# Performance work log

Measured on AMD Instinct MI355X. Metric: run time of the kernel, lower is better.

Reference implementation:

```python
import math
import jax, jax.numpy as jnp
import numpy as np

EPS = 1e-5
NUM_HEADER = 2


def pos_encoding(C, T, dtype):
    i = jnp.arange(C)
    exp = -((i - (i % 2)).astype(dtype) / C)
    freqs = jnp.power(jnp.asarray(10000.0, dtype), exp)[:, None]      # [C,1]
    phases = ((i % 2).astype(dtype) * (np.pi / 2))[:, None]           # [C,1]
    pos = jnp.arange(T, dtype=dtype)[None, :]                         # [1,T]
    return jnp.sin(pos * freqs + phases)                              # [C,T]


def layernorm2d(x, g, b):
    # LayerNorm over (C,T) jointly, per batch element (nn.LayerNorm([C, length]))
    mu = jnp.mean(x, axis=(1, 2), keepdims=True)
    var = jnp.mean((x - mu) ** 2, axis=(1, 2), keepdims=True)
    return (x - mu) * jax.lax.rsqrt(var + EPS) * g[None] + b[None]


def dsconv(x, dw_w, dw_b, pw_w, pw_b):
    # depthwise conv1d (groups=C, 'same' padding for odd k) + pointwise 1x1
    C = x.shape[1]
    k = dw_w.shape[-1]
    y = jax.lax.conv_general_dilated(
        x, dw_w[:, None, :], (1,), [(k // 2, k // 2)],
        dimension_numbers=('NCH', 'OIH', 'NCH'), feature_group_count=C)
    y = y + dw_b[None, :, None]
    y = jnp.einsum('bct,oc->bot', y, pw_w) + pw_b[None, :, None]
    return y


def attention(x, mask, Wq, Wk, Wv, Wo):
    # Faithful to source bug: all heads use Wqs[1]/Wks[1]/Wvs[1] -> identical heads.
    xt = jnp.transpose(x, (0, 2, 1))          # [B,T,C]
    C = xt.shape[-1]
    dk = C / NUM_HEADER
    q = xt @ Wq                               # [B,T,dk]
    k_ = xt @ Wk
    v = xt @ Wv
    s = jnp.einsum('bqd,bkd->bqk', q, k_) * (1.0 / math.sqrt(dk))
    hmask = mask[:, None, :]                  # mask over keys
    s = s * hmask + (1 - hmask) * (-1e30)
    a = jax.nn.softmax(s, axis=2) * mask[:, :, None]
    head = a @ v                              # [B,T,dk]
    heads = jnp.tile(head, (1, 1, NUM_HEADER))  # concat of identical heads
    out = heads @ Wo                          # [B,T,C]
    return jnp.transpose(out, (0, 2, 1))      # [B,C,T]


def setup_inputs() -> dict:
    key = jax.random.key(0)
    B, C, T = 16, 128, 1024
    NCONV, K = 4, 7
    dk = C // NUM_HEADER
    ks = jax.random.split(key, 12)
    inp = {
        'x': jax.random.normal(ks[0], (B, C, T), jnp.float32),
        'mask': jnp.ones((B, T), jnp.float32),
        'dw_w': jax.random.normal(ks[1], (NCONV, C, K), jnp.float32) * math.sqrt(2.0 / K),
        'dw_b': jnp.zeros((NCONV, C), jnp.float32),
        'pw_w': jax.random.normal(ks[2], (NCONV, C, C), jnp.float32) * math.sqrt(2.0 / C),
        'pw_b': jnp.zeros((NCONV, C), jnp.float32),
        'norm0_g': jnp.ones((C, T), jnp.float32),
        'norm0_b': jnp.zeros((C, T), jnp.float32),
        'norms_g': jnp.ones((NCONV, C, T), jnp.float32),
        'norms_b': jnp.zeros((NCONV, C, T), jnp.float32),
        'norme_g': jnp.ones((C, T), jnp.float32),
        'norme_b': jnp.zeros((C, T), jnp.float32),
        'Wq': jax.random.normal(ks[3], (C, dk), jnp.float32) * math.sqrt(2.0 / (C + dk)),
        'Wk': jax.random.normal(ks[4], (C, dk), jnp.float32) * math.sqrt(2.0 / (C + dk)),
        'Wv': jax.random.normal(ks[5], (C, dk), jnp.float32) * math.sqrt(2.0 / (C + dk)),
        'Wo': jax.random.normal(ks[6], (C, C), jnp.float32) * math.sqrt(2.0 / C),
        'fc_w': jax.random.normal(ks[7], (C, C), jnp.float32) * (0.1 * math.sqrt(6.0 / (2 * C))),
        'fc_b': jnp.zeros((C,), jnp.float32),
    }
    return inp


def reference(x, mask, dw_w, dw_b, pw_w, pw_b, norm0_g, norm0_b,
              norms_g, norms_b, norme_g, norme_b,
              Wq, Wk, Wv, Wo, fc_w, fc_b):
    B, C, T = x.shape
    nconv = dw_w.shape[0]
    # dropout is identity in eval mode (reference is deterministic)
    out = x + pos_encoding(C, T, x.dtype)[None]
    res = layernorm2d(out, norm0_g, norm0_b)
    for i in range(nconv):
        out = dsconv(out, dw_w[i], dw_b[i], pw_w[i], pw_b[i])
        out = jax.nn.relu(out)
        out = out + res
        res = out
        out = layernorm2d(out, norms_g[i], norms_b[i])
    out = attention(out, mask, Wq, Wk, Wv, Wo)
    out = out + res
    res = out
    out = layernorm2d(out, norme_g, norme_b)
    out = jnp.einsum('bct,oc->bot', out, fc_w) + fc_b[None, :, None]
    out = jax.nn.relu(out)
    out = out + res
    return out
```

## Files before the change

kernel.cpp:

```cpp
#include <hip/hip_runtime.h>
#include <math.h>

#define BB 16
#define CC 128
#define TT 1024
#define KK 7
#define DK 64
#define NSPLIT 4

typedef float f32x4 __attribute__((ext_vector_type(4)));
typedef short s16x8 __attribute__((ext_vector_type(8)));

__device__ inline short f2bf(float f) {
  union { float f; unsigned u; } v; v.f = f;
  unsigned r = (v.u + 0x7FFFu + ((v.u >> 16) & 1u)) >> 16;
  return (short)r;
}
__device__ inline float bf2f(short s) {
  union { unsigned u; float f; } v;
  v.u = ((unsigned)(unsigned short)s) << 16;
  return v.f;
}

__device__ inline void block_partial_256(float s, float ss, float* dst) {
#pragma unroll
  for (int off = 32; off; off >>= 1) { s += __shfl_xor(s, off); ss += __shfl_xor(ss, off); }
  __shared__ float red[8];
  int w = threadIdx.x >> 6;
  if ((threadIdx.x & 63) == 0) { red[2 * w] = s; red[2 * w + 1] = ss; }
  __syncthreads();
  if (threadIdx.x == 0) {
    for (int i = 1; i < 4; ++i) { s += red[2 * i]; ss += red[2 * i + 1]; }
    dst[0] = s; dst[1] = ss;
  }
}

__device__ inline void ln_stats_from_parts(const float* part_batch, int n, float* sh) {
  if (threadIdx.x < 64) {
    float s = 0.f, ss = 0.f;
    for (int i = threadIdx.x; i < n; i += 64) { s += part_batch[2 * i]; ss += part_batch[2 * i + 1]; }
#pragma unroll
    for (int off = 32; off; off >>= 1) { s += __shfl_xor(s, off); ss += __shfl_xor(ss, off); }
    if (threadIdx.x == 0) {
      const float invN = 1.f / (float)(CC * TT);
      float mu = s * invN;
      sh[0] = mu;
      sh[1] = rsqrtf(ss * invN - mu * mu + 1e-5f);
    }
  }
  __syncthreads();
}

__global__ __launch_bounds__(256) void k_prep_addpos(const float* __restrict__ x,
                                                     const float* __restrict__ pww,
                                                     const float* __restrict__ Wq,
                                                     const float* __restrict__ Wk,
                                                     const float* __restrict__ Wv,
                                                     const float* __restrict__ Wo,
                                                     const float* __restrict__ fcw,
                                                     const float* __restrict__ n0g,
                                                     const float* __restrict__ n0b,
                                                     const float* __restrict__ nsg,
                                                     const float* __restrict__ nsb,
                                                     const float* __restrict__ neg_,
                                                     const float* __restrict__ neb,
                                                     short* __restrict__ out,
                                                     float* __restrict__ part,
                                                     short* __restrict__ pwwb,
                                                     short* __restrict__ wqkvb,
                                                     short* __restrict__ wo2b,
                                                     short* __restrict__ fcwb,
                                                     short* __restrict__ lnpb) {
  if (blockIdx.x < BB * CC) {
    int bc = blockIdx.x;
    int c = bc & (CC - 1);
    float ce = (float)(c & ~1);
    float freq = expf(-(ce / (float)CC) * 9.210340371976184f);
    float phase = (c & 1) ? 1.5707963267948966f : 0.0f;
    const float4* xr = (const float4*)(x + (size_t)bc * TT);
    short* orow = out + (size_t)bc * TT;
    int t = threadIdx.x * 4;
    float4 xv = xr[threadIdx.x];
    float v0 = xv.x + sinf((float)t * freq + phase);
    float v1 = xv.y + sinf((float)(t + 1) * freq + phase);
    float v2 = xv.z + sinf((float)(t + 2) * freq + phase);
    float v3 = xv.w + sinf((float)(t + 3) * freq + phase);
    float s = v0 + v1 + v2 + v3;
    float ss = v0 * v0 + v1 * v1 + v2 * v2 + v3 * v3;
    short4 o; o.x = f2bf(v0); o.y = f2bf(v1); o.z = f2bf(v2); o.w = f2bf(v3);
    *(short4*)(orow + t) = o;
    block_partial_256(s, ss, part + (size_t)bc * 2);
    return;
  }
  int i = (blockIdx.x - BB * CC) * 256 + threadIdx.x;
  if (i < 65536) { pwwb[i] = f2bf(pww[i]); return; }
  i -= 65536;
  if (i < 24576) {
    int m = i >> 7, c = i & 127;
    int sel = m >> 6, d = m & 63;
    const float* srcp = sel == 0 ? Wq : (sel == 1 ? Wk : Wv);
    wqkvb[i] = f2bf(srcp[c * DK + d]);
    return;
  }
  i -= 24576;
  if (i < 8192) {
    int o = i >> 6, d = i & 63;
    wo2b[i] = f2bf(Wo[d * CC + o] + Wo[(d + 64) * CC + o]);
    return;
  }
  i -= 8192;
  if (i < 16384) { fcwb[i] = f2bf(fcw[i]); return; }
  i -= 16384;
  if (i >= 1572864) return;
  const int CT = CC * TT;
  float v;
  if (i < CT) v = n0g[i];
  else if (i < 2 * CT) v = n0b[i - CT];
  else if (i < 6 * CT) v = nsg[i - 2 * CT];
  else if (i < 10 * CT) v = nsb[i - 6 * CT];
  else if (i < 11 * CT) v = neg_[i - 10 * CT];
  else v = neb[i - 11 * CT];
  lnpb[i] = f2bf(v);
}

template <bool LN_IN, bool LN_RES>
__global__ __launch_bounds__(256) void k_dsconv(const short* __restrict__ in,
                                                const short* __restrict__ lng,
                                                const short* __restrict__ lnb,
                                                const float* __restrict__ part_in, int npart,
                                                const float* __restrict__ dww,
                                                const float* __restrict__ dwb,
                                                const short* __restrict__ pwwb,
                                                const float* __restrict__ pwb,
                                                short* __restrict__ out,
                                                float* __restrict__ part_out) {
  int tile = blockIdx.x & 63, b = blockIdx.x >> 6;
  int t0 = tile * 16;
  __shared__ float stats[2];
  __shared__ float xs[CC][33];
  __shared__ __align__(16) short Dt[16][136];
  ln_stats_from_parts(part_in + (size_t)b * npart * 2, npart, stats);
  float mu = stats[0], rs = stats[1];

  for (int ch = threadIdx.x; ch < 512; ch += 256) {
    int c = ch >> 2, half = ch & 3;
    int ts = t0 - 8 + half * 8;
    float v[8];
    if (ts >= 0 && ts < TT) {
      size_t base = ((size_t)b * CC + c) * TT + ts;
      s16x8 raw = *(const s16x8*)(in + base);
      if (LN_IN) {
        s16x8 g = *(const s16x8*)(lng + c * TT + ts);
        s16x8 bb = *(const s16x8*)(lnb + c * TT + ts);
#pragma unroll
        for (int j = 0; j < 8; ++j)
          v[j] = (bf2f(raw[j]) - mu) * rs * bf2f(g[j]) + bf2f(bb[j]);
      } else {
#pragma unroll
        for (int j = 0; j < 8; ++j) v[j] = bf2f(raw[j]);
      }
    } else {
#pragma unroll
      for (int j = 0; j < 8; ++j) v[j] = 0.f;
    }
#pragma unroll
    for (int j = 0; j < 8; ++j) xs[c][half * 8 + j] = v[j];
  }
  __syncthreads();
  for (int i = threadIdx.x; i < 16 * CC; i += 256) {
    int t = i >> 7, c = i & 127;
    float a = dwb[c];
#pragma unroll
    for (int j = 0; j < KK; ++j) a += dww[c * KK + j] * xs[c][t + 5 + j];
    Dt[t][c] = f2bf(a);
  }
  __syncthreads();

  int w = threadIdx.x >> 6, lane = threadIdx.x & 63;
  int lo = lane & 15, hi = lane >> 4;
  f32x4 acc[2];
#pragma unroll
  for (int mt = 0; mt < 2; ++mt) { acc[mt][0] = 0.f; acc[mt][1] = 0.f; acc[mt][2] = 0.f; acc[mt][3] = 0.f; }
#pragma unroll
  for (int ks = 0; ks < 4; ++ks) {
    s16x8 b0 = *(const s16x8*)&Dt[lo][ks * 32 + hi * 8];
    s16x8 a0 = *(const s16x8*)&pwwb[(size_t)(w * 32 + lo) * CC + ks * 32 + hi * 8];
    s16x8 a1 = *(const s16x8*)&pwwb[(size_t)(w * 32 + 16 + lo) * CC + ks * 32 + hi * 8];
    acc[0] = __builtin_amdgcn_mfma_f32_16x16x32_bf16(a0, b0, acc[0], 0, 0, 0);
    acc[1] = __builtin_amdgcn_mfma_f32_16x16x32_bf16(a1, b0, acc[1], 0, 0, 0);
  }

  float s = 0.f, ss = 0.f;
#pragma unroll
  for (int mt = 0; mt < 2; ++mt)
#pragma unroll
    for (int r = 0; r < 4; ++r) {
      int row = w * 32 + mt * 16 + hi * 4 + r;
      int t = t0 + lo;
      float v = acc[mt][r] + pwb[row];
      v = v > 0.f ? v : 0.f;
      size_t idx = ((size_t)b * CC + row) * TT + t;
      float rv = bf2f(in[idx]);
      if (LN_RES) rv = (rv - mu) * rs * bf2f(lng[row * TT + t]) + bf2f(lnb[row * TT + t]);
      v += rv;
      out[idx] = f2bf(v);
      s += v; ss += v * v;
    }
  block_partial_256(s, ss, part_out + (size_t)blockIdx.x * 2);
}

__global__ __launch_bounds__(256) void k_qkv(const short* __restrict__ in,
                                             const short* __restrict__ lng,
                                             const short* __restrict__ lnb,
                                             const float* __restrict__ part_in, int npart,
                                             const short* __restrict__ wqkvb,
                                             short* __restrict__ q,
                                             short* __restrict__ k,
                                             short* __restrict__ vt) {
  int tile = blockIdx.x & 63, b = blockIdx.x >> 6;
  int t0 = tile * 16;
  __shared__ float stats[2];
  __shared__ __align__(16) short Dt[16][136];
  ln_stats_from_parts(part_in + (size_t)b * npart * 2, npart, stats);
  float mu = stats[0], rs = stats[1];
  {
    int i = threadIdx.x;
    int c = i >> 1, half = i & 1;
    int ts = t0 + half * 8;
    size_t base = ((size_t)b * CC + c) * TT + ts;
    s16x8 raw = *(const s16x8*)(in + base);
    s16x8 g = *(const s16x8*)(lng + c * TT + ts);
    s16x8 bb = *(const s16x8*)(lnb + c * TT + ts);
#pragma unroll
    for (int j = 0; j < 8; ++j)
      Dt[half * 8 + j][c] = f2bf((bf2f(raw[j]) - mu) * rs * bf2f(g[j]) + bf2f(bb[j]));
  }
  __syncthreads();

  int w = threadIdx.x >> 6, lane = threadIdx.x & 63;
  int lo = lane & 15, hi = lane >> 4;
  f32x4 acc[3];
#pragma unroll
  for (int mt = 0; mt < 3; ++mt) { acc[mt][0] = 0.f; acc[mt][1] = 0.f; acc[mt][2] = 0.f; acc[mt][3] = 0.f; }
#pragma unroll
  for (int ks = 0; ks < 4; ++ks) {
    s16x8 b0 = *(const s16x8*)&Dt[lo][ks * 32 + hi * 8];
#pragma unroll
    for (int mt = 0; mt < 3; ++mt) {
      s16x8 a = *(const s16x8*)&wqkvb[(size_t)(w * 48 + mt * 16 + lo) * CC + ks * 32 + hi * 8];
      acc[mt] = __builtin_amdgcn_mfma_f32_16x16x32_bf16(a, b0, acc[mt], 0, 0, 0);
    }
  }
#pragma unroll
  for (int mt = 0; mt < 3; ++mt) {
    int m0 = w * 48 + mt * 16 + hi * 4;
    int t = t0 + lo;
    short4 pk;
    pk.x = f2bf(acc[mt][0]); pk.y = f2bf(acc[mt][1]);
    pk.z = f2bf(acc[mt][2]); pk.w = f2bf(acc[mt][3]);
    if (m0 < 64) {
      *(short4*)(q + ((size_t)b * TT + t) * DK + m0) = pk;
    } else if (m0 < 128) {
      *(short4*)(k + ((size_t)b * TT + t) * DK + (m0 - 64)) = pk;
    } else {
      int d = m0 - 128;
      vt[((size_t)b * DK + d) * TT + t] = pk.x;
      vt[((size_t)b * DK + d + 1) * TT + t] = pk.y;
      vt[((size_t)b * DK + d + 2) * TT + t] = pk.z;
      vt[((size_t)b * DK + d + 3) * TT + t] = pk.w;
    }
  }
}

__global__ __launch_bounds__(128) void k_attn(const short* __restrict__ qb,
                                              const short* __restrict__ kbuf,
                                              const short* __restrict__ vtb,
                                              const float* __restrict__ mask,
                                              short* __restrict__ pacc,
                                              float* __restrict__ pml) {
  int sp = blockIdx.x & (NSPLIT - 1);
  int qt = (blockIdx.x >> 2) & 31;
  int b = blockIdx.x >> 7;
  int w = threadIdx.x >> 6, lane = threadIdx.x & 63;
  int lo = lane & 15, hi = lane >> 4;

  __shared__ __align__(16) short ps[2][16][72];

  const short* qp = qb + ((size_t)b * TT + qt * 32 + w * 16 + lo) * DK + hi * 8;
  s16x8 aq0 = *(const s16x8*)qp;
  s16x8 aq1 = *(const s16x8*)(qp + 32);

  f32x4 acc[4];
  float m_i[4], l_i[4];
#pragma unroll
  for (int r = 0; r < 4; ++r) {
    m_i[r] = -3.0e38f; l_i[r] = 0.f;
#pragma unroll
    for (int nt = 0; nt < 4; ++nt) acc[nt][r] = 0.f;
  }
  const float scale = 0.125f;

  for (int kb2 = sp * (TT / 64 / NSPLIT); kb2 < (sp + 1) * (TT / 64 / NSPLIT); ++kb2) {
    f32x4 sc[4];
    float mv[4];
#pragma unroll
    for (int nt = 0; nt < 4; ++nt) {
      const short* kp = kbuf + ((size_t)b * TT + kb2 * 64 + nt * 16 + lo) * DK + hi * 8;
      s16x8 bk0 = *(const s16x8*)kp;
      s16x8 bk1 = *(const s16x8*)(kp + 32);
      f32x4 z; z[0] = 0.f; z[1] = 0.f; z[2] = 0.f; z[3] = 0.f;
      z = __builtin_amdgcn_mfma_f32_16x16x32_bf16(aq0, bk0, z, 0, 0, 0);
      z = __builtin_amdgcn_mfma_f32_16x16x32_bf16(aq1, bk1, z, 0, 0, 0);
      sc[nt] = z;
      mv[nt] = mask[(size_t)b * TT + kb2 * 64 + nt * 16 + lo];
    }
#pragma unroll
    for (int nt = 0; nt < 4; ++nt) {
      float addv = (1.f - mv[nt]) * -1e30f;
#pragma unroll
      for (int r = 0; r < 4; ++r) sc[nt][r] = sc[nt][r] * scale * mv[nt] + addv;
    }
    float alpha[4];
#pragma unroll
    for (int r = 0; r < 4; ++r) {
      float m0 = fmaxf(fmaxf(sc[0][r], sc[1][r]), fmaxf(sc[2][r], sc[3][r]));
#pragma unroll
      for (int off = 1; off < 16; off <<= 1) m0 = fmaxf(m0, __shfl_xor(m0, off));
      float mn = fmaxf(m_i[r], m0);
      alpha[r] = __expf(m_i[r] - mn);
      m_i[r] = mn;
    }
    float psum[4] = {0.f, 0.f, 0.f, 0.f};
#pragma unroll
    for (int nt = 0; nt < 4; ++nt)
#pragma unroll
      for (int r = 0; r < 4; ++r) {
        float p = __expf(sc[nt][r] - m_i[r]);
        psum[r] += p;
        ps[w][hi * 4 + r][nt * 16 + lo] = f2bf(p);
      }
#pragma unroll
    for (int r = 0; r < 4; ++r) {
      float sum = psum[r];
#pragma unroll
      for (int off = 1; off < 16; off <<= 1) sum += __shfl_xor(sum, off);
      l_i[r] = l_i[r] * alpha[r] + sum;
    }
#pragma unroll
    for (int nt = 0; nt < 4; ++nt)
#pragma unroll
      for (int r = 0; r < 4; ++r) acc[nt][r] *= alpha[r];

    s16x8 ap0 = *(const s16x8*)&ps[w][lo][hi * 8];
    s16x8 ap1 = *(const s16x8*)&ps[w][lo][32 + hi * 8];
#pragma unroll
    for (int nt = 0; nt < 4; ++nt) {
      const short* vp = vtb + ((size_t)b * DK + nt * 16 + lo) * TT + kb2 * 64 + hi * 8;
      s16x8 bv0 = *(const s16x8*)vp;
      s16x8 bv1 = *(const s16x8*)(vp + 32);
      acc[nt] = __builtin_amdgcn_mfma_f32_16x16x32_bf16(ap0, bv0, acc[nt], 0, 0, 0);
      acc[nt] = __builtin_amdgcn_mfma_f32_16x16x32_bf16(ap1, bv1, acc[nt], 0, 0, 0);
    }
  }
#pragma unroll
  for (int r = 0; r < 4; ++r) {
    int row = qt * 32 + w * 16 + hi * 4 + r;
    size_t pb = (((size_t)b * TT + row) * NSPLIT + sp) * DK;
#pragma unroll
    for (int nt = 0; nt < 4; ++nt) pacc[pb + nt * 16 + lo] = f2bf(acc[nt][r]);
    if (lo == 0) {
      size_t mb = (((size_t)b * TT + row) * NSPLIT + sp) * 2;
      pml[mb] = m_i[r];
      pml[mb + 1] = l_i[r];
    }
  }
}

__global__ __launch_bounds__(256) void k_attnout(const short* __restrict__ pacc,
                                                 const float* __restrict__ pml,
                                                 const float* __restrict__ mask,
                                                 const short* __restrict__ wo2b,
                                                 const short* __restrict__ res,
                                                 short* __restrict__ out,
                                                 float* __restrict__ part_out) {
  int tile = blockIdx.x & 63, b = blockIdx.x >> 6;
  int t0 = tile * 16;
  __shared__ __align__(16) short Ht[16][72];
  if (threadIdx.x < 128) {
    int row = threadIdx.x >> 3, d8 = threadIdx.x & 7;
    size_t rb = (size_t)b * TT + t0 + row;
    float m[NSPLIT], l[NSPLIT];
#pragma unroll
    for (int s = 0; s < NSPLIT; ++s) {
      m[s] = pml[(rb * NSPLIT + s) * 2];
      l[s] = pml[(rb * NSPLIT + s) * 2 + 1];
    }
    float M = fmaxf(fmaxf(m[0], m[1]), fmaxf(m[2], m[3]));
    float wgt[NSPLIT], L = 0.f;
#pragma unroll
    for (int s = 0; s < NSPLIT; ++s) { wgt[s] = __expf(m[s] - M); L += wgt[s] * l[s]; }
    float inv = mask[rb] / L;
    float o[8];
#pragma unroll
    for (int j = 0; j < 8; ++j) o[j] = 0.f;
#pragma unroll
    for (int s = 0; s < NSPLIT; ++s) {
      s16x8 pv = *(const s16x8*)(pacc + (rb * NSPLIT + s) * DK + d8 * 8);
#pragma unroll
      for (int j = 0; j < 8; ++j) o[j] += wgt[s] * bf2f(pv[j]);
    }
    s16x8 hv;
#pragma unroll
    for (int j = 0; j < 8; ++j) hv[j] = f2bf(o[j] * inv);
    *(s16x8*)&Ht[row][d8 * 8] = hv;
  }
  __syncthreads();

  int w = threadIdx.x >> 6, lane = threadIdx.x & 63;
  int lo = lane & 15, hi = lane >> 4;
  f32x4 acc[2];
#pragma unroll
  for (int mt = 0; mt < 2; ++mt) { acc[mt][0] = 0.f; acc[mt][1] = 0.f; acc[mt][2] = 0.f; acc[mt][3] = 0.f; }
#pragma unroll
  for (int ks = 0; ks < 2; ++ks) {
    s16x8 b0 = *(const s16x8*)&Ht[lo][ks * 32 + hi * 8];
    s16x8 a0 = *(const s16x8*)&wo2b[(size_t)(w * 32 + lo) * DK + ks * 32 + hi * 8];
    s16x8 a1 = *(const s16x8*)&wo2b[(size_t)(w * 32 + 16 + lo) * DK + ks * 32 + hi * 8];
    acc[0] = __builtin_amdgcn_mfma_f32_16x16x32_bf16(a0, b0, acc[0], 0, 0, 0);
    acc[1] = __builtin_amdgcn_mfma_f32_16x16x32_bf16(a1, b0, acc[1], 0, 0, 0);
  }
  float s = 0.f, ss = 0.f;
#pragma unroll
  for (int mt = 0; mt < 2; ++mt)
#pragma unroll
    for (int r = 0; r < 4; ++r) {
      int row = w * 32 + mt * 16 + hi * 4 + r;
      int t = t0 + lo;
      size_t idx = ((size_t)b * CC + row) * TT + t;
      float v = acc[mt][r] + bf2f(res[idx]);
      out[idx] = f2bf(v);
      s += v; ss += v * v;
    }
  block_partial_256(s, ss, part_out + (size_t)blockIdx.x * 2);
}

__global__ __launch_bounds__(256) void k_fc(const short* __restrict__ in,
                                            const short* __restrict__ lng,
                                            const short* __restrict__ lnb,
                                            const float* __restrict__ part_in, int npart,
                                            const short* __restrict__ fcwb,
                                            const float* __restrict__ fb,
                                            float* __restrict__ out) {
  int tile = blockIdx.x & 63, b = blockIdx.x >> 6;
  int t0 = tile * 16;
  __shared__ float stats[2];
  __shared__ __align__(16) short Dt[16][136];
  ln_stats_from_parts(part_in + (size_t)b * npart * 2, npart, stats);
  float mu = stats[0], rs = stats[1];
  {
    int i = threadIdx.x;
    int c = i >> 1, half = i & 1;
    int ts = t0 + half * 8;
    size_t base = ((size_t)b * CC + c) * TT + ts;
    s16x8 raw = *(const s16x8*)(in + base);
    s16x8 g = *(const s16x8*)(lng + c * TT + ts);
    s16x8 bb = *(const s16x8*)(lnb + c * TT + ts);
#pragma unroll
    for (int j = 0; j < 8; ++j)
      Dt[half * 8 + j][c] = f2bf((bf2f(raw[j]) - mu) * rs * bf2f(g[j]) + bf2f(bb[j]));
  }
  __syncthreads();

  int w = threadIdx.x >> 6, lane = threadIdx.x & 63;
  int lo = lane & 15, hi = lane >> 4;
  f32x4 acc[2];
#pragma unroll
  for (int mt = 0; mt < 2; ++mt) { acc[mt][0] = 0.f; acc[mt][1] = 0.f; acc[mt][2] = 0.f; acc[mt][3] = 0.f; }
#pragma unroll
  for (int ks = 0; ks < 4; ++ks) {
    s16x8 b0 = *(const s16x8*)&Dt[lo][ks * 32 + hi * 8];
    s16x8 a0 = *(const s16x8*)&fcwb[(size_t)(w * 32 + lo) * CC + ks * 32 + hi * 8];
    s16x8 a1 = *(const s16x8*)&fcwb[(size_t)(w * 32 + 16 + lo) * CC + ks * 32 + hi * 8];
    acc[0] = __builtin_amdgcn_mfma_f32_16x16x32_bf16(a0, b0, acc[0], 0, 0, 0);
    acc[1] = __builtin_amdgcn_mfma_f32_16x16x32_bf16(a1, b0, acc[1], 0, 0, 0);
  }
#pragma unroll
  for (int mt = 0; mt < 2; ++mt)
#pragma unroll
    for (int r = 0; r < 4; ++r) {
      int row = w * 32 + mt * 16 + hi * 4 + r;
      int t = t0 + lo;
      size_t idx = ((size_t)b * CC + row) * TT + t;
      float v = acc[mt][r] + fb[row];
      v = v > 0.f ? v : 0.f;
      out[idx] = v + bf2f(in[idx]);
    }
}

extern "C" void kernel_launch(void* const* d_in, const int* in_sizes, int n_in,
                              void* d_out, int out_size, void* d_ws, size_t ws_size,
                              hipStream_t stream) {
  const float* x    = (const float*)d_in[0];
  const float* mask = (const float*)d_in[1];
  const float* dww  = (const float*)d_in[2];
  const float* dwb  = (const float*)d_in[3];
  const float* pww  = (const float*)d_in[4];
  const float* pwb  = (const float*)d_in[5];
  const float* n0g  = (const float*)d_in[6];
  const float* n0b  = (const float*)d_in[7];
  const float* nsg  = (const float*)d_in[8];
  const float* nsb  = (const float*)d_in[9];
  const float* neg_ = (const float*)d_in[10];
  const float* neb  = (const float*)d_in[11];
  const float* Wq   = (const float*)d_in[12];
  const float* Wk   = (const float*)d_in[13];
  const float* Wv   = (const float*)d_in[14];
  const float* Wo   = (const float*)d_in[15];
  const float* fcw  = (const float*)d_in[16];
  const float* fcb  = (const float*)d_in[17];
  float* out = (float*)d_out;

  float* W = (float*)d_ws;
  const size_t NBCT = (size_t)BB * CC * TT;
  const size_t NBTD = (size_t)BB * TT * DK;
  const size_t CT = (size_t)CC * TT;
  float* PART0 = W;
  float* PARTS = W + 4096;
  float* PML   = W + 4096 + 5 * 2048;
  short* OB    = (short*)(PML + 131072);
  short* SB    = OB + NBCT;
  short* QB    = SB + NBCT;
  short* KB    = QB + NBTD;
  short* VT    = KB + NBTD;
  short* PACC  = VT + NBTD;
  short* PWWB  = PACC + NBTD * NSPLIT;
  short* WQKVB = PWWB + 65536;
  short* WO2B  = WQKVB + 24576;
  short* FCWB  = WO2B + 8192;
  short* LNPB  = FCWB + 16384;
  short* N0G = LNPB, *N0B = LNPB + CT;
  short* NSG0 = LNPB + 2 * CT;
  short* NSB0 = LNPB + 6 * CT;
  short* NEG = LNPB + 10 * CT, *NEB = LNPB + 11 * CT;

  k_prep_addpos<<<BB * CC + 6592, 256, 0, stream>>>(
      x, pww, Wq, Wk, Wv, Wo, fcw, n0g, n0b, nsg, nsb, neg_, neb,
      OB, PART0, PWWB, WQKVB, WO2B, FCWB, LNPB);
  k_dsconv<false, true><<<BB * 64, 256, 0, stream>>>(
      OB, N0G, N0B, PART0, 128, dww, dwb, PWWB, pwb, SB, PARTS);
  k_dsconv<true, false><<<BB * 64, 256, 0, stream>>>(
      SB, NSG0, NSB0, PARTS, 64,
      dww + 1 * CC * KK, dwb + 1 * CC, PWWB + 1 * CC * CC, pwb + 1 * CC, OB, PARTS + 2048);
  k_dsconv<true, false><<<BB * 64, 256, 0, stream>>>(
      OB, NSG0 + CT, NSB0 + CT, PARTS + 2048, 64,
      dww + 2 * CC * KK, dwb + 2 * CC, PWWB + 2 * CC * CC, pwb + 2 * CC, SB, PARTS + 4096);
  k_dsconv<true, false><<<BB * 64, 256, 0, stream>>>(
      SB, NSG0 + 2 * CT, NSB0 + 2 * CT, PARTS + 4096, 64,
      dww + 3 * CC * KK, dwb + 3 * CC, PWWB + 3 * CC * CC, pwb + 3 * CC, OB, PARTS + 6144);
  k_qkv<<<BB * 64, 256, 0, stream>>>(OB, NSG0 + 3 * CT, NSB0 + 3 * CT, PARTS + 6144, 64,
                                     WQKVB, QB, KB, VT);
  k_attn<<<BB * 32 * NSPLIT, 128, 0, stream>>>(QB, KB, VT, mask, PACC, PML);
  k_attnout<<<BB * 64, 256, 0, stream>>>(PACC, PML, mask, WO2B, OB, SB, PARTS + 8192);
  k_fc<<<BB * 64, 256, 0, stream>>>(SB, NEG, NEB, PARTS + 8192, 64, FCWB, fcb, out);
}
```

Baseline: 219.8 us.

## Fuse all pipeline stages into one persistent kernel with grid barriers

Replaces the nine separate kernel launches with a single persistent kernel of 512 blocks. The stages are separated by software grid barriers built on atomic counters, which are cleared by a memset before launch. LayerNorm gamma and beta are now read directly as fp32 instead of being pre-converted to bf16, which removes a large conversion pass from the prep stage. Each block handles two tiles per stage. This removes launch gaps and the conversion work, but adds spin-wait barrier overhead, assumes every block is co-resident, and adds a memset call.

```diff
diff --git a/kernel.cpp b/kernel.cpp
--- a/kernel.cpp
+++ b/kernel.cpp
@@ -7,6 +7,7 @@
 #define KK 7
 #define DK 64
 #define NSPLIT 4
+#define NBLK 512
 
 typedef float f32x4 __attribute__((ext_vector_type(4)));
 typedef short s16x8 __attribute__((ext_vector_type(8)));
@@ -20,6 +21,25 @@
   union { unsigned u; float f; } v;
   v.u = ((unsigned)(unsigned short)s) << 16;
   return v.f;
+}
+
+__device__ inline void grid_barrier(unsigned* barr, int k) {
+  __syncthreads();
+  if (threadIdx.x == 0) {
+    __threadfence();
+    unsigned prev = __hip_atomic_fetch_add(&barr[2 * k], 1u, __ATOMIC_ACQ_REL,
+                                           __HIP_MEMORY_SCOPE_AGENT);
+    if (prev == NBLK - 1) {
+      __hip_atomic_store(&barr[2 * k + 1], 1u, __ATOMIC_RELEASE, __HIP_MEMORY_SCOPE_AGENT);
+    } else {
+      while (__hip_atomic_load(&barr[2 * k + 1], __ATOMIC_ACQUIRE,
+                               __HIP_MEMORY_SCOPE_AGENT) == 0u) {
+        __builtin_amdgcn_s_sleep(8);
+      }
+    }
+    __threadfence();
+  }
+  __syncthreads();
 }
 
 __device__ inline void block_partial_256(float s, float ss, float* dst) {
@@ -51,110 +71,40 @@
   __syncthreads();
 }
 
-__global__ __launch_bounds__(256) void k_prep_addpos(const float* __restrict__ x,
-                                                     const float* __restrict__ pww,
-                                                     const float* __restrict__ Wq,
-                                                     const float* __restrict__ Wk,
-                                                     const float* __restrict__ Wv,
-                                                     const float* __restrict__ Wo,
-                                                     const float* __restrict__ fcw,
-                                                     const float* __restrict__ n0g,
-                                                     const float* __restrict__ n0b,
-                                                     const float* __restrict__ nsg,
-                                                     const float* __restrict__ nsb,
-                                                     const float* __restrict__ neg_,
-                                                     const float* __restrict__ neb,
-                                                     short* __restrict__ out,
-                                                     float* __restrict__ part,
-                                                     short* __restrict__ pwwb,
-                                                     short* __restrict__ wqkvb,
-                                                     short* __restrict__ wo2b,
-                                                     short* __restrict__ fcwb,
-                                                     short* __restrict__ lnpb) {
-  if (blockIdx.x < BB * CC) {
-    int bc = blockIdx.x;
-    int c = bc & (CC - 1);
-    float ce = (float)(c & ~1);
-    float freq = expf(-(ce / (float)CC) * 9.210340371976184f);
-    float phase = (c & 1) ? 1.5707963267948966f : 0.0f;
-    const float4* xr = (const float4*)(x + (size_t)bc * TT);
-    short* orow = out + (size_t)bc * TT;
-    int t = threadIdx.x * 4;
-    float4 xv = xr[threadIdx.x];
-    float v0 = xv.x + sinf((float)t * freq + phase);
-    float v1 = xv.y + sinf((float)(t + 1) * freq + phase);
-    float v2 = xv.z + sinf((float)(t + 2) * freq + phase);
-    float v3 = xv.w + sinf((float)(t + 3) * freq + phase);
-    float s = v0 + v1 + v2 + v3;
-    float ss = v0 * v0 + v1 * v1 + v2 * v2 + v3 * v3;
-    short4 o; o.x = f2bf(v0); o.y = f2bf(v1); o.z = f2bf(v2); o.w = f2bf(v3);
-    *(short4*)(orow + t) = o;
-    block_partial_256(s, ss, part + (size_t)bc * 2);
-    return;
-  }
-  int i = (blockIdx.x - BB * CC) * 256 + threadIdx.x;
-  if (i < 65536) { pwwb[i] = f2bf(pww[i]); return; }
-  i -= 65536;
-  if (i < 24576) {
-    int m = i >> 7, c = i & 127;
-    int sel = m >> 6, d = m & 63;
-    const float* srcp = sel == 0 ? Wq : (sel == 1 ? Wk : Wv);
-    wqkvb[i] = f2bf(srcp[c * DK + d]);
-    return;
-  }
-  i -= 24576;
-  if (i < 8192) {
-    int o = i >> 6, d = i & 63;
-    wo2b[i] = f2bf(Wo[d * CC + o] + Wo[(d + 64) * CC + o]);
-    return;
-  }
-  i -= 8192;
-  if (i < 16384) { fcwb[i] = f2bf(fcw[i]); return; }
-  i -= 16384;
-  if (i >= 1572864) return;
-  const int CT = CC * TT;
-  float v;
-  if (i < CT) v = n0g[i];
-  else if (i < 2 * CT) v = n0b[i - CT];
-  else if (i < 6 * CT) v = nsg[i - 2 * CT];
-  else if (i < 10 * CT) v = nsb[i - 6 * CT];
-  else if (i < 11 * CT) v = neg_[i - 10 * CT];
-  else v = neb[i - 11 * CT];
-  lnpb[i] = f2bf(v);
-}
-
-template <bool LN_IN, bool LN_RES>
-__global__ __launch_bounds__(256) void k_dsconv(const short* __restrict__ in,
-                                                const short* __restrict__ lng,
-                                                const short* __restrict__ lnb,
-                                                const float* __restrict__ part_in, int npart,
-                                                const float* __restrict__ dww,
-                                                const float* __restrict__ dwb,
-                                                const short* __restrict__ pwwb,
-                                                const float* __restrict__ pwb,
-                                                short* __restrict__ out,
-                                                float* __restrict__ part_out) {
-  int tile = blockIdx.x & 63, b = blockIdx.x >> 6;
+struct MegaP {
+  const float *x, *mask, *dww, *dwb, *pww, *pwb;
+  const float *n0g, *n0b, *nsg, *nsb, *neg, *neb;
+  const float *Wq, *Wk, *Wv, *Wo, *fcw, *fcb;
+  float* out;
+  float *part0, *parts, *pml;
+  short *ob, *sb, *qb, *kb, *vt, *pacc;
+  short *pwwb, *wqkvb, *wo2b, *fcwb;
+  unsigned* barr;
+};
+
+__device__ void dsconv_tile(const short* __restrict__ in,
+                            const float* __restrict__ lng, const float* __restrict__ lnb,
+                            const float* __restrict__ dww, const float* __restrict__ dwb,
+                            const short* __restrict__ pwwb, const float* __restrict__ pwb,
+                            short* __restrict__ outp, float* __restrict__ partdst,
+                            bool LN_IN, bool LN_RES, int tile, int b, float mu, float rs,
+                            float (*xs)[33], short (*Dt)[136]) {
   int t0 = tile * 16;
-  __shared__ float stats[2];
-  __shared__ float xs[CC][33];
-  __shared__ __align__(16) short Dt[16][136];
-  ln_stats_from_parts(part_in + (size_t)b * npart * 2, npart, stats);
-  float mu = stats[0], rs = stats[1];
-
   for (int ch = threadIdx.x; ch < 512; ch += 256) {
     int c = ch >> 2, half = ch & 3;
     int ts = t0 - 8 + half * 8;
     float v[8];
     if (ts >= 0 && ts < TT) {
-      size_t base = ((size_t)b * CC + c) * TT + ts;
-      s16x8 raw = *(const s16x8*)(in + base);
+      s16x8 raw = *(const s16x8*)(in + ((size_t)b * CC + c) * TT + ts);
       if (LN_IN) {
-        s16x8 g = *(const s16x8*)(lng + c * TT + ts);
-        s16x8 bb = *(const s16x8*)(lnb + c * TT + ts);
-#pragma unroll
-        for (int j = 0; j < 8; ++j)
-          v[j] = (bf2f(raw[j]) - mu) * rs * bf2f(g[j]) + bf2f(bb[j]);
+        float4 g0 = *(const float4*)(lng + c * TT + ts);
+        float4 g1 = *(const float4*)(lng + c * TT + ts + 4);
+        float4 b0 = *(const float4*)(lnb + c * TT + ts);
+        float4 b1 = *(const float4*)(lnb + c * TT + ts + 4);
+        float gg[8] = {g0.x, g0.y, g0.z, g0.w, g1.x, g1.y, g1.z, g1.w};
+        float bb[8] = {b0.x, b0.y, b0.z, b0.w, b1.x, b1.y, b1.z, b1.w};
+#pragma unroll
+        for (int j = 0; j < 8; ++j) v[j] = (bf2f(raw[j]) - mu) * rs * gg[j] + bb[j];
       } else {
 #pragma unroll
         for (int j = 0; j < 8; ++j) v[j] = bf2f(raw[j]);
@@ -189,7 +139,6 @@
     acc[0] = __builtin_amdgcn_mfma_f32_16x16x32_bf16(a0, b0, acc[0], 0, 0, 0);
     acc[1] = __builtin_amdgcn_mfma_f32_16x16x32_bf16(a1, b0, acc[1], 0, 0, 0);
   }
-
   float s = 0.f, ss = 0.f;
 #pragma unroll
   for (int mt = 0; mt < 2; ++mt)
@@ -201,365 +150,423 @@
       v = v > 0.f ? v : 0.f;
       size_t idx = ((size_t)b * CC + row) * TT + t;
       float rv = bf2f(in[idx]);
-      if (LN_RES) rv = (rv - mu) * rs * bf2f(lng[row * TT + t]) + bf2f(lnb[row * TT + t]);
+      if (LN_RES) rv = (rv - mu) * rs * lng[row * TT + t] + lnb[row * TT + t];
       v += rv;
-      out[idx] = f2bf(v);
+      outp[idx] = f2bf(v);
       s += v; ss += v * v;
     }
-  block_partial_256(s, ss, part_out + (size_t)blockIdx.x * 2);
-}
-
-__global__ __launch_bounds__(256) void k_qkv(const short* __restrict__ in,
-                                             const short* __restrict__ lng,
-                                             const short* __restrict__ lnb,
-                                             const float* __restrict__ part_in, int npart,
-                                             const short* __restrict__ wqkvb,
-                                             short* __restrict__ q,
-                                             short* __restrict__ k,
-                                             short* __restrict__ vt) {
-  int tile = blockIdx.x & 63, b = blockIdx.x >> 6;
-  int t0 = tile * 16;
-  __shared__ float stats[2];
-  __shared__ __align__(16) short Dt[16][136];
-  ln_stats_from_parts(part_in + (size_t)b * npart * 2, npart, stats);
-  float mu = stats[0], rs = stats[1];
+  block_partial_256(s, ss, partdst);
+  __syncthreads();
+}
+
+__device__ void stage_dsconv(const MegaP& P, const short* in,
+                             const float* lng, const float* lnb,
+                             const float* part_in, int npart,
+                             const float* dww, const float* dwb,
+                             const short* pwwb, const float* pwb,
+                             short* outp, float* part_out,
+                             bool LN_IN, bool LN_RES,
+                             float* s_stats, float (*xs)[33], short (*Dt)[136]) {
+  int b = blockIdx.x >> 5, tg = blockIdx.x & 31;
+  ln_stats_from_parts(part_in + (size_t)b * npart * 2, npart, s_stats);
+  float mu = s_stats[0], rs = s_stats[1];
+  __syncthreads();
+  for (int tt = 0; tt < 2; ++tt) {
+    int tile = tg * 2 + tt;
+    dsconv_tile(in, lng, lnb, dww, dwb, pwwb, pwb, outp,
+                part_out + ((size_t)b * 64 + tg * 2 + tt) * 2,
+                LN_IN, LN_RES, tile, b, mu, rs, xs, Dt);
+  }
+}
+
+__global__ __launch_bounds__(256, 2) void k_mega(MegaP P) {
+  const int CT = CC * TT;
+  __shared__ __align__(16) char smraw[21504];
+  float* s_stats = (float*)smraw;
+  float (*s_xs)[33] = (float(*)[33])(smraw + 16);
+  short (*s_Dt)[136] = (short(*)[136])(smraw + 16 + 16896);
+  short (*s_DtG)[136] = (short(*)[136])(smraw + 16);
+  short (*s_ps)[16][72] = (short(*)[16][72])smraw;
+  short (*s_Ht)[72] = (short(*)[72])smraw;
+
   {
-    int i = threadIdx.x;
-    int c = i >> 1, half = i & 1;
-    int ts = t0 + half * 8;
-    size_t base = ((size_t)b * CC + c) * TT + ts;
-    s16x8 raw = *(const s16x8*)(in + base);
-    s16x8 g = *(const s16x8*)(lng + c * TT + ts);
-    s16x8 bb = *(const s16x8*)(lnb + c * TT + ts);
-#pragma unroll
-    for (int j = 0; j < 8; ++j)
-      Dt[half * 8 + j][c] = f2bf((bf2f(raw[j]) - mu) * rs * bf2f(g[j]) + bf2f(bb[j]));
-  }
-  __syncthreads();
-
-  int w = threadIdx.x >> 6, lane = threadIdx.x & 63;
-  int lo = lane & 15, hi = lane >> 4;
-  f32x4 acc[3];
-#pragma unroll
-  for (int mt = 0; mt < 3; ++mt) { acc[mt][0] = 0.f; acc[mt][1] = 0.f; acc[mt][2] = 0.f; acc[mt][3] = 0.f; }
-#pragma unroll
-  for (int ks = 0; ks < 4; ++ks) {
-    s16x8 b0 = *(const s16x8*)&Dt[lo][ks * 32 + hi * 8];
-#pragma unroll
-    for (int mt = 0; mt < 3; ++mt) {
-      s16x8 a = *(const s16x8*)&wqkvb[(size_t)(w * 48 + mt * 16 + lo) * CC + ks * 32 + hi * 8];
-      acc[mt] = __builtin_amdgcn_mfma_f32_16x16x32_bf16(a, b0, acc[mt], 0, 0, 0);
-    }
-  }
-#pragma unroll
-  for (int mt = 0; mt < 3; ++mt) {
-    int m0 = w * 48 + mt * 16 + hi * 4;
-    int t = t0 + lo;
-    short4 pk;
-    pk.x = f2bf(acc[mt][0]); pk.y = f2bf(acc[mt][1]);
-    pk.z = f2bf(acc[mt][2]); pk.w = f2bf(acc[mt][3]);
-    if (m0 < 64) {
-      *(short4*)(q + ((size_t)b * TT + t) * DK + m0) = pk;
-    } else if (m0 < 128) {
-      *(short4*)(k + ((size_t)b * TT + t) * DK + (m0 - 64)) = pk;
-    } else {
-      int d = m0 - 128;
-      vt[((size_t)b * DK + d) * TT + t] = pk.x;
-      vt[((size_t)b * DK + d + 1) * TT + t] = pk.y;
-      vt[((size_t)b * DK + d + 2) * TT + t] = pk.z;
-      vt[((size_t)b * DK + d + 3) * TT + t] = pk.w;
-    }
-  }
-}
-
-__global__ __launch_bounds__(128) void k_attn(const short* __restrict__ qb,
-                                              const short* __restrict__ kbuf,
-                                              const short* __restrict__ vtb,
-                                              const float* __restrict__ mask,
-                                              short* __restrict__ pacc,
-                                              float* __restrict__ pml) {
-  int sp = blockIdx.x & (NSPLIT - 1);
-  int qt = (blockIdx.x >> 2) & 31;
-  int b = blockIdx.x >> 7;
-  int w = threadIdx.x >> 6, lane = threadIdx.x & 63;
-  int lo = lane & 15, hi = lane >> 4;
-
-  __shared__ __align__(16) short ps[2][16][72];
-
-  const short* qp = qb + ((size_t)b * TT + qt * 32 + w * 16 + lo) * DK + hi * 8;
-  s16x8 aq0 = *(const s16x8*)qp;
-  s16x8 aq1 = *(const s16x8*)(qp + 32);
-
-  f32x4 acc[4];
-  float m_i[4], l_i[4];
-#pragma unroll
-  for (int r = 0; r < 4; ++r) {
-    m_i[r] = -3.0e38f; l_i[r] = 0.f;
-#pragma unroll
-    for (int nt = 0; nt < 4; ++nt) acc[nt][r] = 0.f;
-  }
-  const float scale = 0.125f;
-
-  for (int kb2 = sp * (TT / 64 / NSPLIT); kb2 < (sp + 1) * (TT / 64 / NSPLIT); ++kb2) {
-    f32x4 sc[4];
-    float mv[4];
-#pragma unroll
-    for (int nt = 0; nt < 4; ++nt) {
-      const short* kp = kbuf + ((size_t)b * TT + kb2 * 64 + nt * 16 + lo) * DK + hi * 8;
-      s16x8 bk0 = *(const s16x8*)kp;
-      s16x8 bk1 = *(const s16x8*)(kp + 32);
-      f32x4 z; z[0] = 0.f; z[1] = 0.f; z[2] = 0.f; z[3] = 0.f;
-      z = __builtin_amdgcn_mfma_f32_16x16x32_bf16(aq0, bk0, z, 0, 0, 0);
-      z = __builtin_amdgcn_mfma_f32_16x16x32_bf16(aq1, bk1, z, 0, 0, 0);
-      sc[nt] = z;
-      mv[nt] = mask[(size_t)b * TT + kb2 * 64 + nt * 16 + lo];
-    }
-#pragma unroll
-    for (int nt = 0; nt < 4; ++nt) {
-      float addv = (1.f - mv[nt]) * -1e30f;
-#pragma unroll
-      for (int r = 0; r < 4; ++r) sc[nt][r] = sc[nt][r] * scale * mv[nt] + addv;
-    }
-    float alpha[4];
+    int i = blockIdx.x * 256 + threadIdx.x;
+    if (i < 65536) { P.pwwb[i] = f2bf(P.pww[i]); }
+    else if (i < 90112) {
+      int j = i - 65536; int m = j >> 7, c = j & 127;
+      int sel = m >> 6, d = m & 63;
+      const float* sp2 = sel == 0 ? P.Wq : (sel == 1 ? P.Wk : P.Wv);
+      P.wqkvb[j] = f2bf(sp2[c * DK + d]);
+    } else if (i < 98304) {
+      int j = i - 90112; int o = j >> 6, d = j & 63;
+      P.wo2b[j] = f2bf(P.Wo[d * CC + o] + P.Wo[(d + 64) * CC + o]);
+    } else if (i < 114688) {
+      int j = i - 98304; P.fcwb[j] = f2bf(P.fcw[j]);
+    }
+    for (int rr = 0; rr < 4; ++rr) {
+      int bc = blockIdx.x * 4 + rr;
+      int c = bc & (CC - 1);
+      float ce = (float)(c & ~1);
+      float freq = expf(-(ce / (float)CC) * 9.210340371976184f);
+      float phase = (c & 1) ? 1.5707963267948966f : 0.0f;
+      const float4* xr = (const float4*)(P.x + (size_t)bc * TT);
+      short* orow = P.ob + (size_t)bc * TT;
+      int t = threadIdx.x * 4;
+      float4 xv = xr[threadIdx.x];
+      float v0 = xv.x + sinf((float)t * freq + phase);
+      float v1 = xv.y + sinf((float)(t + 1) * freq + phase);
+      float v2 = xv.z + sinf((float)(t + 2) * freq + phase);
+      float v3 = xv.w + sinf((float)(t + 3) * freq + phase);
+      float s = v0 + v1 + v2 + v3;
+      float ss = v0 * v0 + v1 * v1 + v2 * v2 + v3 * v3;
+      short4 o4; o4.x = f2bf(v0); o4.y = f2bf(v1); o4.z = f2bf(v2); o4.w = f2bf(v3);
+      *(short4*)(orow + t) = o4;
+      block_partial_256(s, ss, P.part0 + (size_t)bc * 2);
+      __syncthreads();
+    }
+  }
+  grid_barrier(P.barr, 0);
+
+  stage_dsconv(P, P.ob, P.n0g, P.n0b, P.part0, 128, P.dww, P.dwb, P.pwwb, P.pwb,
+               P.sb, P.parts, false, true, s_stats, s_xs, s_Dt);
+  grid_barrier(P.barr, 1);
+  stage_dsconv(P, P.sb, P.nsg, P.nsb, P.parts, 64,
+               P.dww + CC * KK, P.dwb + CC, P.pwwb + CC * CC, P.pwb + CC,
+               P.ob, P.parts + 2048, true, false, s_stats, s_xs, s_Dt);
+  grid_barrier(P.barr, 2);
+  stage_dsconv(P, P.ob, P.nsg + CT, P.nsb + CT, P.parts + 2048, 64,
+               P.dww + 2 * CC * KK, P.dwb + 2 * CC, P.pwwb + 2 * CC * CC, P.pwb + 2 * CC,
+               P.sb, P.parts + 4096, true, false, s_stats, s_xs, s_Dt);
+  grid_barrier(P.barr, 3);
+  stage_dsconv(P, P.sb, P.nsg + 2 * CT, P.nsb + 2 * CT, P.parts + 4096, 64,
+               P.dww + 3 * CC * KK, P.dwb + 3 * CC, P.pwwb + 3 * CC * CC, P.pwb + 3 * CC,
+               P.ob, P.parts + 6144, true, false, s_stats, s_xs, s_Dt);
+  grid_barrier(P.barr, 4);
+
+  {
+    int b = blockIdx.x >> 5, tg = blockIdx.x & 31;
+    const float* lng = P.nsg + 3 * CT;
+    const float* lnb = P.nsb + 3 * CT;
+    ln_stats_from_parts(P.parts + 6144 + (size_t)b * 128, 64, s_stats);
+    float mu = s_stats[0], rs = s_stats[1];
+    __syncthreads();
+    for (int tt = 0; tt < 2; ++tt) {
+      int t0 = (tg * 2 + tt) * 16;
+      {
+        int i = threadIdx.x;
+        int c = i >> 1, half = i & 1;
+        int ts = t0 + half * 8;
+        s16x8 raw = *(const s16x8*)(P.ob + ((size_t)b * CC + c) * TT + ts);
+        float4 g0 = *(const float4*)(lng + c * TT + ts);
+        float4 g1 = *(const float4*)(lng + c * TT + ts + 4);
+        float4 b0 = *(const float4*)(lnb + c * TT + ts);
+        float4 b1 = *(const float4*)(lnb + c * TT + ts + 4);
+        float gg[8] = {g0.x, g0.y, g0.z, g0.w, g1.x, g1.y, g1.z, g1.w};
+        float bb[8] = {b0.x, b0.y, b0.z, b0.w, b1.x, b1.y, b1.z, b1.w};
+#pragma unroll
+        for (int j = 0; j < 8; ++j)
+          s_DtG[half * 8 + j][c] = f2bf((bf2f(raw[j]) - mu) * rs * gg[j] + bb[j]);
+      }
+      __syncthreads();
+      int w = threadIdx.x >> 6, lane = threadIdx.x & 63;
+      int lo = lane & 15, hi = lane >> 4;
+      f32x4 acc[3];
+#pragma unroll
+      for (int mt = 0; mt < 3; ++mt) { acc[mt][0] = 0.f; acc[mt][1] = 0.f; acc[mt][2] = 0.f; acc[mt][3] = 0.f; }
+#pragma unroll
+      for (int ks = 0; ks < 4; ++ks) {
+        s16x8 b0 = *(const s16x8*)&s_DtG[lo][ks * 32 + hi * 8];
+#pragma unroll
+        for (int mt = 0; mt < 3; ++mt) {
+          s16x8 a = *(const s16x8*)&P.wqkvb[(size_t)(w * 48 + mt * 16 + lo) * CC + ks * 32 + hi * 8];
+          acc[mt] = __builtin_amdgcn_mfma_f32_16x16x32_bf16(a, b0, acc[mt], 0, 0, 0);
+        }
+      }
+#pragma unroll
+      for (int mt = 0; mt < 3; ++mt) {
+        int m0 = w * 48 + mt * 16 + hi * 4;
+        int t = t0 + lo;
+        short4 pk;
+        pk.x = f2bf(acc[mt][0]); pk.y = f2bf(acc[mt][1]);
+        pk.z = f2bf(acc[mt][2]); pk.w = f2bf(acc[mt][3]);
+        if (m0 < 64) {
+          *(short4*)(P.qb + ((size_t)b * TT + t) * DK + m0) = pk;
+        } else if (m0 < 128) {
+          *(short4*)(P.kb + ((size_t)b * TT + t) * DK + (m0 - 64)) = pk;
+        } else {
+          int d = m0 - 128;
+          P.vt[((size_t)b * DK + d) * TT + t] = pk.x;
+          P.vt[((size_t)b * DK + d + 1) * TT + t] = pk.y;
+          P.vt[((size_t)b * DK + d + 2) * TT + t] = pk.z;
+          P.vt[((size_t)b * DK + d + 3) * TT + t] = pk.w;
+        }
+      }
+      __syncthreads();
+    }
+  }
+  grid_barrier(P.barr, 5);
+
+  for (int iter = 0; iter < 2; ++iter) {
+    int gu = blockIdx.x * 2 + (threadIdx.x >> 7) + iter * 1024;
+    int sp = gu & (NSPLIT - 1);
+    int qt = (gu >> 2) & 31;
+    int b = gu >> 7;
+    int w = threadIdx.x >> 6;
+    int wq = w & 1;
+    int lane = threadIdx.x & 63;
+    int lo = lane & 15, hi = lane >> 4;
+
+    const short* qp = P.qb + ((size_t)b * TT + qt * 32 + wq * 16 + lo) * DK + hi * 8;
+    s16x8 aq0 = *(const s16x8*)qp;
+    s16x8 aq1 = *(const s16x8*)(qp + 32);
+
+    f32x4 acc[4];
+    float m_i[4], l_i[4];
 #pragma unroll
     for (int r = 0; r < 4; ++r) {
-      float m0 = fmaxf(fmaxf(sc[0][r], sc[1][r]), fmaxf(sc[2][r], sc[3][r]));
-#pragma unroll
-      for (int off = 1; off < 16; off <<= 1) m0 = fmaxf(m0, __shfl_xor(m0, off));
-      float mn = fmaxf(m_i[r], m0);
-      alpha[r] = __expf(m_i[r] - mn);
-      m_i[r] = mn;
-    }
-    float psum[4] = {0.f, 0.f, 0.f, 0.f};
-#pragma unroll
-    for (int nt = 0; nt < 4; ++nt)
+      m_i[r] = -3.0e38f; l_i[r] = 0.f;
+#pragma unroll
+      for (int nt = 0; nt < 4; ++nt) acc[nt][r] = 0.f;
+    }
+    const float scale = 0.125f;
+
+    for (int kb2 = sp * (TT / 64 / NSPLIT); kb2 < (sp + 1) * (TT / 64 / NSPLIT); ++kb2) {
+      f32x4 sc[4];
+      float mv[4];
+#pragma unroll
+      for (int nt = 0; nt < 4; ++nt) {
+        const short* kp = P.kb + ((size_t)b * TT + kb2 * 64 + nt * 16 + lo) * DK + hi * 8;
+        s16x8 bk0 = *(const s16x8*)kp;
+        s16x8 bk1 = *(const s16x8*)(kp + 32);
+        f32x4 z; z[0] = 0.f; z[1] = 0.f; z[2] = 0.f; z[3] = 0.f;
+        z = __builtin_amdgcn_mfma_f32_16x16x32_bf16(aq0, bk0, z, 0, 0, 0);
+        z = __builtin_amdgcn_mfma_f32_16x16x32_bf16(aq1, bk1, z, 0, 0, 0);
+        sc[nt] = z;
+        mv[nt] = P.mask[(size_t)b * TT + kb2 * 64 + nt * 16 + lo];
+      }
+#pragma unroll
+      for (int nt = 0; nt < 4; ++nt) {
+        float addv = (1.f - mv[nt]) * -1e30f;
+#pragma unroll
+        for (int r = 0; r < 4; ++r) sc[nt][r] = sc[nt][r] * scale * mv[nt] + addv;
+      }
+      float alpha[4];
 #pragma unroll
       for (int r = 0; r < 4; ++r) {
-        float p = __expf(sc[nt][r] - m_i[r]);
-        psum[r] += p;
-        ps[w][hi * 4 + r][nt * 16 + lo] = f2bf(p);
-      }
+        float m0 = fmaxf(fmaxf(sc[0][r], sc[1][r]), fmaxf(sc[2][r], sc[3][r]));
+#pragma unroll
+        for (int off = 1; off < 16; off <<= 1) m0 = fmaxf(m0, __shfl_xor(m0, off));
+        float mn = fmaxf(m_i[r], m0);
+        alpha[r] = __expf(m_i[r] - mn);
+        m_i[r] = mn;
+      }
+      float psum[4] = {0.f, 0.f, 0.f, 0.f};
+#pragma unroll
+      for (int nt = 0; nt < 4; ++nt)
+#pragma unroll
+        for (int r = 0; r < 4; ++r) {
+          float p = __expf(sc[nt][r] - m_i[r]);
+          psum[r] += p;
+          s_ps[w][hi * 4 + r][nt * 16 + lo] = f2bf(p);
+        }
+#pragma unroll
+      for (int r = 0; r < 4; ++r) {
+        float sum = psum[r];
+#pragma unroll
+        for (int off = 1; off < 16; off <<= 1) sum += __shfl_xor(sum, off);
+        l_i[r] = l_i[r] * alpha[r] + sum;
+      }
+#pragma unroll
+      for (int nt = 0; nt < 4; ++nt)
+#pragma unroll
+        for (int r = 0; r < 4; ++r) acc[nt][r] *= alpha[r];
+
+      s16x8 ap0 = *(const s16x8*)&s_ps[w][lo][hi * 8];
+      s16x8 ap1 = *(const s16x8*)&s_ps[w][lo][32 + hi * 8];
+#pragma unroll
+      for (int nt = 0; nt < 4; ++nt) {
+        const short* vp = P.vt + ((size_t)b * DK + nt * 16 + lo) * TT + kb2 * 64 + hi * 8;
+        s16x8 bv0 = *(const s16x8*)vp;
+        s16x8 bv1 = *(const s16x8*)(vp + 32);
+        acc[nt] = __builtin_amdgcn_mfma_f32_16x16x32_bf16(ap0, bv0, acc[nt], 0, 0, 0);
+        acc[nt] = __builtin_amdgcn_mfma_f32_16x16x32_bf16(ap1, bv1, acc[nt], 0, 0, 0);
+      }
+    }
 #pragma unroll
     for (int r = 0; r < 4; ++r) {
-      float sum = psum[r];
-#pragma unroll
-      for (int off = 1; off < 16; off <<= 1) sum += __shfl_xor(sum, off);
-      l_i[r] = l_i[r] * alpha[r] + sum;
-    }
-#pragma unroll
-    for (int nt = 0; nt < 4; ++nt)
-#pragma unroll
-      for (int r = 0; r < 4; ++r) acc[nt][r] *= alpha[r];
-
-    s16x8 ap0 = *(const s16x8*)&ps[w][lo][hi * 8];
-    s16x8 ap1 = *(const s16x8*)&ps[w][lo][32 + hi * 8];
-#pragma unroll
-    for (int nt = 0; nt < 4; ++nt) {
-      const short* vp = vtb + ((size_t)b * DK + nt * 16 + lo) * TT + kb2 * 64 + hi * 8;
-      s16x8 bv0 = *(const s16x8*)vp;
-      s16x8 bv1 = *(const s16x8*)(vp + 32);
-      acc[nt] = __builtin_amdgcn_mfma_f32_16x16x32_bf16(ap0, bv0, acc[nt], 0, 0, 0);
-      acc[nt] = __builtin_amdgcn_mfma_f32_16x16x32_bf16(ap1, bv1, acc[nt], 0, 0, 0);
-    }
-  }
-#pragma unroll
-  for (int r = 0; r < 4; ++r) {
-    int row = qt * 32 + w * 16 + hi * 4 + r;
-    size_t pb = (((size_t)b * TT + row) * NSPLIT + sp) * DK;
-#pragma unroll
-    for (int nt = 0; nt < 4; ++nt) pacc[pb + nt * 16 + lo] = f2bf(acc[nt][r]);
-    if (lo == 0) {
-      size_t mb = (((size_t)b * TT + row) * NSPLIT + sp) * 2;
-      pml[mb] = m_i[r];
-      pml[mb + 1] = l_i[r];
-    }
-  }
-}
-
-__global__ __launch_bounds__(256) void k_attnout(const short* __restrict__ pacc,
-                                                 const float* __restrict__ pml,
-                                                 const float* __restrict__ mask,
-                                                 const short* __restrict__ wo2b,
-                                                 const short* __restrict__ res,
-                                                 short* __restrict__ out,
-                                                 float* __restrict__ part_out) {
-  int tile = blockIdx.x & 63, b = blockIdx.x >> 6;
-  int t0 = tile * 16;
-  __shared__ __align__(16) short Ht[16][72];
-  if (threadIdx.x < 128) {
-    int row = threadIdx.x >> 3, d8 = threadIdx.x & 7;
-    size_t rb = (size_t)b * TT + t0 + row;
-    float m[NSPLIT], l[NSPLIT];
-#pragma unroll
-    for (int s = 0; s < NSPLIT; ++s) {
-      m[s] = pml[(rb * NSPLIT + s) * 2];
-      l[s] = pml[(rb * NSPLIT + s) * 2 + 1];
-    }
-    float M = fmaxf(fmaxf(m[0], m[1]), fmaxf(m[2], m[3]));
-    float wgt[NSPLIT], L = 0.f;
-#pragma unroll
-    for (int s = 0; s < NSPLIT; ++s) { wgt[s] = __expf(m[s] - M); L += wgt[s] * l[s]; }
-    float inv = mask[rb] / L;
-    float o[8];
-#pragma unroll
-    for (int j = 0; j < 8; ++j) o[j] = 0.f;
-#pragma unroll
-    for (int s = 0; s < NSPLIT; ++s) {
-      s16x8 pv = *(const s16x8*)(pacc + (rb * NSPLIT + s) * DK + d8 * 8);
-#pragma unroll
-      for (int j = 0; j < 8; ++j) o[j] += wgt[s] * bf2f(pv[j]);
-    }
-    s16x8 hv;
-#pragma unroll
-    for (int j = 0; j < 8; ++j) hv[j] = f2bf(o[j] * inv);
-    *(s16x8*)&Ht[row][d8 * 8] = hv;
-  }
-  __syncthreads();
-
-  int w = threadIdx.x >> 6, lane = threadIdx.x & 63;
-  int lo = lane & 15, hi = lane >> 4;
-  f32x4 acc[2];
-#pragma unroll
-  for (int mt = 0; mt < 2; ++mt) { acc[mt][0] = 0.f; acc[mt][1] = 0.f; acc[mt][2] = 0.f; acc[mt][3] = 0.f; }
-#pragma unroll
-  for (int ks = 0; ks < 2; ++ks) {
-    s16x8 b0 = *(const s16x8*)&Ht[lo][ks * 32 + hi * 8];
-    s16x8 a0 = *(const s16x8*)&wo2b[(size_t)(w * 32 + lo) * DK + ks * 32 + hi * 8];
-    s16x8 a1 = *(const s16x8*)&wo2b[(size_t)(w * 32 + 16 + lo) * DK + ks * 32 + hi * 8];
-    acc[0] = __builtin_amdgcn_mfma_f32_16x16x32_bf16(a0, b0, acc[0], 0, 0, 0);
-    acc[1] = __builtin_amdgcn_mfma_f32_16x16x32_bf16(a1, b0, acc[1], 0, 0, 0);
-  }
-  float s = 0.f, ss = 0.f;
-#pragma unroll
-  for (int mt = 0; mt < 2; ++mt)
-#pragma unroll
-    for (int r = 0; r < 4; ++r) {
-      int row = w * 32 + mt * 16 + hi * 4 + r;
-      int t = t0 + lo;
-      size_t idx = ((size_t)b * CC + row) * TT + t;
-      float v = acc[mt][r] + bf2f(res[idx]);
-      out[idx] = f2bf(v);
-      s += v; ss += v * v;
-    }
-  block_partial_256(s, ss, part_out + (size_t)blockIdx.x * 2);
-}
-
-__global__ __launch_bounds__(256) void k_fc(const short* __restrict__ in,
-                                            const short* __restrict__ lng,
-                                            const short* __restrict__ lnb,
-                                            const float* __restrict__ part_in, int npart,
-                                            const short* __restrict__ fcwb,
-                                            const float* __restrict__ fb,
-                                            float* __restrict__ out) {
-  int tile = blockIdx.x & 63, b = blockIdx.x >> 6;
-  int t0 = tile * 16;
-  __shared__ float stats[2];
-  __shared__ __align__(16) short Dt[16][136];
-  ln_stats_from_parts(part_in + (size_t)b * npart * 2, npart, stats);
-  float mu = stats[0], rs = stats[1];
+      int row = qt * 32 + wq * 16 + hi * 4 + r;
+      size_t pb = (((size_t)b * TT + row) * NSPLIT + sp) * DK;
+#pragma unroll
+      for (int nt = 0; nt < 4; ++nt) P.pacc[pb + nt * 16 + lo] = f2bf(acc[nt][r]);
+      if (lo == 0) {
+        size_t mb = (((size_t)b * TT + row) * NSPLIT + sp) * 2;
+        P.pml[mb] = m_i[r];
+        P.pml[mb + 1] = l_i[r];
+      }
+    }
+  }
+  grid_barrier(P.barr, 6);
+
   {
-    int i = threadIdx.x;
-    int c = i >> 1, half = i & 1;
-    int ts = t0 + half * 8;
-    size_t base = ((size_t)b * CC + c) * TT + ts;
-    s16x8 raw = *(const s16x8*)(in + base);
-    s16x8 g = *(const s16x8*)(lng + c * TT + ts);
-    s16x8 bb = *(const s16x8*)(lnb + c * TT + ts);
-#pragma unroll
-    for (int j = 0; j < 8; ++j)
-      Dt[half * 8 + j][c] = f2bf((bf2f(raw[j]) - mu) * rs * bf2f(g[j]) + bf2f(bb[j]));
-  }
-  __syncthreads();
-
-  int w = threadIdx.x >> 6, lane = threadIdx.x & 63;
-  int lo = lane & 15, hi = lane >> 4;
-  f32x4 acc[2];
-#pragma unroll
-  for (int mt = 0; mt < 2; ++mt) { acc[mt][0] = 0.f; acc[mt][1] = 0.f; acc[mt][2] = 0.f; acc[mt][3] = 0.f; }
-#pragma unroll
-  for (int ks = 0; ks < 4; ++ks) {
-    s16x8 b0 = *(const s16x8*)&Dt[lo][ks * 32 + hi * 8];
-    s16x8 a0 = *(const s16x8*)&fcwb[(size_t)(w * 32 + lo) * CC + ks * 32 + hi * 8];
-    s16x8 a1 = *(const s16x8*)&fcwb[(size_t)(w * 32 + 16 + lo) * CC + ks * 32 + hi * 8];
-    acc[0] = __builtin_amdgcn_mfma_f32_16x16x32_bf16(a0, b0, acc[0], 0, 0, 0);
-    acc[1] = __builtin_amdgcn_mfma_f32_16x16x32_bf16(a1, b0, acc[1], 0, 0, 0);
-  }
-#pragma unroll
-  for (int mt = 0; mt < 2; ++mt)
-#pragma unroll
-    for (int r = 0; r < 4; ++r) {
-      int row = w * 32 + mt * 16 + hi * 4 + r;
-      int t = t0 + lo;
-      size_t idx = ((size_t)b * CC + row) * TT + t;
-      float v = acc[mt][r] + fb[row];
-      v = v > 0.f ? v : 0.f;
-      out[idx] = v + bf2f(in[idx]);
-    }
+    int b = blockIdx.x >> 5, tg = blockIdx.x & 31;
+    for (int tt = 0; tt < 2; ++tt) {
+      int t0 = (tg * 2 + tt) * 16;
+      if (threadIdx.x < 128) {
+        int row = threadIdx.x >> 3, d8 = threadIdx.x & 7;
+        size_t rb = (size_t)b * TT + t0 + row;
+        float m[NSPLIT], l[NSPLIT];
+#pragma unroll
+        for (int s = 0; s < NSPLIT; ++s) {
+          m[s] = P.pml[(rb * NSPLIT + s) * 2];
+          l[s] = P.pml[(rb * NSPLIT + s) * 2 + 1];
+        }
+        float M = fmaxf(fmaxf(m[0], m[1]), fmaxf(m[2], m[3]));
+        float wgt[NSPLIT], L = 0.f;
+#pragma unroll
+        for (int s = 0; s < NSPLIT; ++s) { wgt[s] = __expf(m[s] - M); L += wgt[s] * l[s]; }
+        float inv = P.mask[rb] / L;
+        float o[8];
+#pragma unroll
+        for (int j = 0; j < 8; ++j) o[j] = 0.f;
+#pragma unroll
+        for (int s = 0; s < NSPLIT; ++s) {
+          s16x8 pv = *(const s16x8*)(P.pacc + (rb * NSPLIT + s) * DK + d8 * 8);
+#pragma unroll
+          for (int j = 0; j < 8; ++j) o[j] += wgt[s] * bf2f(pv[j]);
+        }
+        s16x8 hv;
+#pragma unroll
+        for (int j = 0; j < 8; ++j) hv[j] = f2bf(o[j] * inv);
+        *(s16x8*)&s_Ht[row][d8 * 8] = hv;
+      }
+      __syncthreads();
+
+      int w = threadIdx.x >> 6, lane = threadIdx.x & 63;
+      int lo = lane & 15, hi = lane >> 4;
+      f32x4 acc[2];
+#pragma unroll
+      for (int mt = 0; mt < 2; ++mt) { acc[mt][0] = 0.f; acc[mt][1] = 0.f; acc[mt][2] = 0.f; acc[mt][3] = 0.f; }
+#pragma unroll
+      for (int ks = 0; ks < 2; ++ks) {
+        s16x8 b0 = *(const s16x8*)&s_Ht[lo][ks * 32 + hi * 8];
+        s16x8 a0 = *(const s16x8*)&P.wo2b[(size_t)(w * 32 + lo) * DK + ks * 32 + hi * 8];
+        s16x8 a1 = *(const s16x8*)&P.wo2b[(size_t)(w * 32 + 16 + lo) * DK + ks * 32 + hi * 8];
+        acc[0] = __builtin_amdgcn_mfma_f32_16x16x32_bf16(a0, b0, acc[0], 0, 0, 0);
+        acc[1] = __builtin_amdgcn_mfma_f32_16x16x32_bf16(a1, b0, acc[1], 0, 0, 0);
+      }
+      float s = 0.f, ss = 0.f;
+#pragma unroll
+      for (int mt = 0; mt < 2; ++mt)
+#pragma unroll
+        for (int r = 0; r < 4; ++r) {
+          int row = w * 32 + mt * 16 + hi * 4 + r;
+          int t = t0 + lo;
+          size_t idx = ((size_t)b * CC + row) * TT + t;
+          float v = acc[mt][r] + bf2f(P.ob[idx]);
+          P.sb[idx] = f2bf(v);
+          s += v; ss += v * v;
+        }
+      block_partial_256(s, ss, P.parts + 8192 + ((size_t)b * 64 + tg * 2 + tt) * 2);
+      __syncthreads();
+    }
+  }
+  grid_barrier(P.barr, 7);
+
+  {
+    int b = blockIdx.x >> 5, tg = blockIdx.x & 31;
+    ln_stats_from_parts(P.parts + 8192 + (size_t)b * 128, 64, s_stats);
+    float mu = s_stats[0], rs = s_stats[1];
+    __syncthreads();
+    for (int tt = 0; tt < 2; ++tt) {
+      int t0 = (tg * 2 + tt) * 16;
+      {
+        int i = threadIdx.x;
+        int c = i >> 1, half = i & 1;
+        int ts = t0 + half * 8;
+        s16x8 raw = *(const s16x8*)(P.sb + ((size_t)b * CC + c) * TT + ts);
+        float4 g0 = *(const float4*)(P.neg + c * TT + ts);
+        float4 g1 = *(const float4*)(P.neg + c * TT + ts + 4);
+        float4 b0 = *(const float4*)(P.neb + c * TT + ts);
+        float4 b1 = *(const float4*)(P.neb + c * TT + ts + 4);
+        float gg[8] = {g0.x, g0.y, g0.z, g0.w, g1.x, g1.y, g1.z, g1.w};
+        float bb[8] = {b0.x, b0.y, b0.z, b0.w, b1.x, b1.y, b1.z, b1.w};
+#pragma unroll
+        for (int j = 0; j < 8; ++j)
+          s_DtG[half * 8 + j][c] = f2bf((bf2f(raw[j]) - mu) * rs * gg[j] + bb[j]);
+      }
+      __syncthreads();
+
+      int w = threadIdx.x >> 6, lane = threadIdx.x & 63;
+      int lo = lane & 15, hi = lane >> 4;
+      f32x4 acc[2];
+#pragma unroll
+      for (int mt = 0; mt < 2; ++mt) { acc[mt][0] = 0.f; acc[mt][1] = 0.f; acc[mt][2] = 0.f; acc[mt][3] = 0.f; }
+#pragma unroll
+      for (int ks = 0; ks < 4; ++ks) {
+        s16x8 b0 = *(const s16x8*)&s_DtG[lo][ks * 32 + hi * 8];
+        s16x8 a0 = *(const s16x8*)&P.fcwb[(size_t)(w * 32 + lo) * CC + ks * 32 + hi * 8];
+        s16x8 a1 = *(const s16x8*)&P.fcwb[(size_t)(w * 32 + 16 + lo) * CC + ks * 32 + hi * 8];
+        acc[0] = __builtin_amdgcn_mfma_f32_16x16x32_bf16(a0, b0, acc[0], 0, 0, 0);
+        acc[1] = __builtin_amdgcn_mfma_f32_16x16x32_bf16(a1, b0, acc[1], 0, 0, 0);
+      }
+#pragma unroll
+      for (int mt = 0; mt < 2; ++mt)
+#pragma unroll
+        for (int r = 0; r < 4; ++r) {
+          int row = w * 32 + mt * 16 + hi * 4 + r;
+          int t = t0 + lo;
+          size_t idx = ((size_t)b * CC + row) * TT + t;
+          float v = acc[mt][r] + P.fcb[row];
+          v = v > 0.f ? v : 0.f;
+          P.out[idx] = v + bf2f(P.sb[idx]);
+        }
+      __syncthreads();
+    }
+  }
 }
 
 extern "C" void kernel_launch(void* const* d_in, const int* in_sizes, int n_in,
                               void* d_out, int out_size, void* d_ws, size_t ws_size,
                               hipStream_t stream) {
-  const float* x    = (const float*)d_in[0];
-  const float* mask = (const float*)d_in[1];
-  const float* dww  = (const float*)d_in[2];
-  const float* dwb  = (const float*)d_in[3];
-  const float* pww  = (const float*)d_in[4];
-  const float* pwb  = (const float*)d_in[5];
-  const float* n0g  = (const float*)d_in[6];
-  const float* n0b  = (const float*)d_in[7];
-  const float* nsg  = (const float*)d_in[8];
-  const float* nsb  = (const float*)d_in[9];
-  const float* neg_ = (const float*)d_in[10];
-  const float* neb  = (const float*)d_in[11];
-  const float* Wq   = (const float*)d_in[12];
-  const float* Wk   = (const float*)d_in[13];
-  const float* Wv   = (const float*)d_in[14];
-  const float* Wo   = (const float*)d_in[15];
-  const float* fcw  = (const float*)d_in[16];
-  const float* fcb  = (const float*)d_in[17];
-  float* out = (float*)d_out;
+  MegaP P;
+  P.x    = (const float*)d_in[0];
+  P.mask = (const float*)d_in[1];
+  P.dww  = (const float*)d_in[2];
+  P.dwb  = (const float*)d_in[3];
+  P.pww  = (const float*)d_in[4];
+  P.pwb  = (const float*)d_in[5];
+  P.n0g  = (const float*)d_in[6];
+  P.n0b  = (const float*)d_in[7];
+  P.nsg  = (const float*)d_in[8];
+  P.nsb  = (const float*)d_in[9];
+  P.neg  = (const float*)d_in[10];
+  P.neb  = (const float*)d_in[11];
+  P.Wq   = (const float*)d_in[12];
+  P.Wk   = (const float*)d_in[13];
+  P.Wv   = (const float*)d_in[14];
+  P.Wo   = (const float*)d_in[15];
+  P.fcw  = (const float*)d_in[16];
+  P.fcb  = (const float*)d_in[17];
+  P.out  = (float*)d_out;
 
   float* W = (float*)d_ws;
   const size_t NBCT = (size_t)BB * CC * TT;
   const size_t NBTD = (size_t)BB * TT * DK;
-  const size_t CT = (size_t)CC * TT;
-  float* PART0 = W;
-  float* PARTS = W + 4096;
-  float* PML   = W + 4096 + 5 * 2048;
-  short* OB    = (short*)(PML + 131072);
-  short* SB    = OB + NBCT;
-  short* QB    = SB + NBCT;
-  short* KB    = QB + NBTD;
-  short* VT    = KB + NBTD;
-  short* PACC  = VT + NBTD;
-  short* PWWB  = PACC + NBTD * NSPLIT;
-  short* WQKVB = PWWB + 65536;
-  short* WO2B  = WQKVB + 24576;
-  short* FCWB  = WO2B + 8192;
-  short* LNPB  = FCWB + 16384;
-  short* N0G = LNPB, *N0B = LNPB + CT;
-  short* NSG0 = LNPB + 2 * CT;
-  short* NSB0 = LNPB + 6 * CT;
-  short* NEG = LNPB + 10 * CT, *NEB = LNPB + 11 * CT;
-
-  k_prep_addpos<<<BB * CC + 6592, 256, 0, stream>>>(
-      x, pww, Wq, Wk, Wv, Wo, fcw, n0g, n0b, nsg, nsb, neg_, neb,
-      OB, PART0, PWWB, WQKVB, WO2B, FCWB, LNPB);
-  k_dsconv<false, true><<<BB * 64, 256, 0, stream>>>(
-      OB, N0G, N0B, PART0, 128, dww, dwb, PWWB, pwb, SB, PARTS);
-  k_dsconv<true, false><<<BB * 64, 256, 0, stream>>>(
-      SB, NSG0, NSB0, PARTS, 64,
-      dww + 1 * CC * KK, dwb + 1 * CC, PWWB + 1 * CC * CC, pwb + 1 * CC, OB, PARTS + 2048);
-  k_dsconv<true, false><<<BB * 64, 256, 0, stream>>>(
-      OB, NSG0 + CT, NSB0 + CT, PARTS + 2048, 64,
-      dww + 2 * CC * KK, dwb + 2 * CC, PWWB + 2 * CC * CC, pwb + 2 * CC, SB, PARTS + 4096);
-  k_dsconv<true, false><<<BB * 64, 256, 0, stream>>>(
-      SB, NSG0 + 2 * CT, NSB0 + 2 * CT, PARTS + 4096, 64,
-      dww + 3 * CC * KK, dwb + 3 * CC, PWWB + 3 * CC * CC, pwb + 3 * CC, OB, PARTS + 6144);
-  k_qkv<<<BB * 64, 256, 0, stream>>>(OB, NSG0 + 3 * CT, NSB0 + 3 * CT, PARTS + 6144, 64,
-                                     WQKVB, QB, KB, VT);
-  k_attn<<<BB * 32 * NSPLIT, 128, 0, stream>>>(QB, KB, VT, mask, PACC, PML);
-  k_attnout<<<BB * 64, 256, 0, stream>>>(PACC, PML, mask, WO2B, OB, SB, PARTS + 8192);
-  k_fc<<<BB * 64, 256, 0, stream>>>(SB, NEG, NEB, PARTS + 8192, 64, FCWB, fcb, out);
-}
+  P.part0 = W;
+  P.parts = W + 4096;
+  P.pml   = W + 4096 + 5 * 2048;
+  P.ob    = (short*)(P.pml + 131072);
+  P.sb    = P.ob + NBCT;
+  P.qb    = P.sb + NBCT;
+  P.kb    = P.qb + NBTD;
+  P.vt    = P.kb + NBTD;
+  P.pacc  = P.vt + NBTD;
+  P.pwwb  = P.pacc + NBTD * NSPLIT;
+  P.wqkvb = P.pwwb + 65536;
+  P.wo2b  = P.wqkvb + 24576;
+  P.fcwb  = P.wo2b + 8192;
+  P.barr  = (unsigned*)(P.fcwb + 16384);
+
+  hipMemsetAsync(P.barr, 0, 64, stream);
+  k_mega<<<NBLK, 256, 0, stream>>>(P);
+}
```

Result: slower. 672.2 us (+205.9%).
